# Kernel optimization log

Measured on AMD Instinct MI355X. Metric: run time of the kernel, lower is better.

Reference implementation:

```python
import jax, jax.numpy as jnp
import numpy as np

B, S, D, H = 2, 2048, 1024, 16
HD = D // H  # head_dim = 64


def setup_inputs() -> dict:
    key = jax.random.key(0)
    ks = jax.random.split(key, 5)
    scale = 1.0 / np.sqrt(D)
    return {
        "x": jax.random.normal(ks[0], (B, S, D), dtype=jnp.float32),
        "attention_mask": jnp.zeros((B, 1, 1, S), dtype=jnp.float32),
        "Wq": jax.random.normal(ks[1], (D, D), dtype=jnp.float32) * scale,
        "Wk": jax.random.normal(ks[2], (D, D), dtype=jnp.float32) * scale,
        "Wv": jax.random.normal(ks[3], (D, D), dtype=jnp.float32) * scale,
        "Wo": jax.random.normal(ks[4], (D, D), dtype=jnp.float32) * scale,
    }


def reference(x, attention_mask, Wq, Wk, Wv, Wo):
    # nn.Linear applies x @ W.T; weights here stored as [out, in]
    q = jnp.einsum("bsd,ed->bse", x, Wq).reshape(B, S, H, HD).transpose(0, 2, 1, 3)
    k = jnp.einsum("bsd,ed->bse", x, Wk).reshape(B, S, H, HD).transpose(0, 2, 1, 3)
    v = jnp.einsum("bsd,ed->bse", x, Wv).reshape(B, S, H, HD).transpose(0, 2, 1, 3)
    scores = jnp.einsum("bhqd,bhkd->bhqk", q, k) / jnp.sqrt(jnp.float32(HD))
    scores = scores + attention_mask  # additive mask, broadcasts [B,1,1,S]
    attn = jax.nn.softmax(scores, axis=-1)  # dropout p=0 (eval) -> identity
    ctx = jnp.einsum("bhqk,bhkd->bhqd", attn, v)
    ctx = ctx.transpose(0, 2, 1, 3).reshape(B, S, D)
    out = jnp.einsum("bsd,ed->bse", ctx, Wo)
    return out
```

## Files before the change

kernel.cpp:

```cpp
#include <hip/hip_runtime.h>
#include <hip/hip_bf16.h>
#include <cstdint>
#include <cstddef>


#define B_  2
#define S_  2048
#define D_  1024
#define H_  16
#define HD_ 64

typedef __bf16 bf16x8 __attribute__((ext_vector_type(8)));
typedef __bf16 bf16x4 __attribute__((ext_vector_type(4)));
typedef float  f32x4  __attribute__((ext_vector_type(4)));

__device__ __forceinline__ void async16(const __bf16* g, const __bf16* l) {
  __builtin_amdgcn_global_load_lds(
      (const __attribute__((address_space(1))) void*)(uintptr_t)g,
      (__attribute__((address_space(3))) void*)(uint32_t)(uintptr_t)l,
      16, 0, 0);
}

__global__ __launch_bounds__(256) void cvt_all(const float* __restrict__ x,
    const float* __restrict__ wq, const float* __restrict__ wk,
    const float* __restrict__ wv, const float* __restrict__ wo,
    __bf16* __restrict__ xb, __bf16* __restrict__ wqb, __bf16* __restrict__ wkb,
    __bf16* __restrict__ wvb, __bf16* __restrict__ wob) {
  const int sel = blockIdx.y;
  const float* src; __bf16* dst; int n;
  if      (sel == 0) { src = x;  dst = xb;  n = B_ * S_ * D_; }
  else if (sel == 1) { src = wq; dst = wqb; n = D_ * D_; }
  else if (sel == 2) { src = wk; dst = wkb; n = D_ * D_; }
  else if (sel == 3) { src = wv; dst = wvb; n = D_ * D_; }
  else               { src = wo; dst = wob; n = D_ * D_; }
  for (int i = blockIdx.x * 256 + threadIdx.x; i * 4 < n; i += gridDim.x * 256) {
    const float4 v = *(const float4*)(src + (size_t)i * 4);
    bf16x4 o;
    o[0] = (__bf16)v.x; o[1] = (__bf16)v.y; o[2] = (__bf16)v.z; o[3] = (__bf16)v.w;
    *(bf16x4*)(dst + (size_t)i * 4) = o;
  }
}

template <typename TC>
__device__ __forceinline__ void gemm97_body(const __bf16* __restrict__ A,
                                            const __bf16* __restrict__ Bm,
                                            TC* __restrict__ C,
                                            const int m0, const int n0,
                                            const int N, const int K) {
  __shared__ __align__(16) __bf16 As[128 * 64];
  __shared__ __align__(16) __bf16 Bs[128 * 64];
  const int tid  = threadIdx.x, lane = tid & 63, wave = tid >> 6;
  const int l15  = lane & 15,   quad = lane >> 4;
  const int wr   = wave >> 1,   wc   = wave & 1;
  const int ebase = wave * 2048 + lane * 8;

  f32x4 acc[4][4] = {};
  for (int k0 = 0; k0 < K; k0 += 64) {
#pragma unroll
    for (int i = 0; i < 4; ++i) {
      const int e = ebase + i * 512;
      const int row = e >> 6, col = e & 63;
      async16(A  + (size_t)(m0 + row) * K + k0 + col, As + (wave * 4 + i) * 512);
      async16(Bm + (size_t)(n0 + row) * K + k0 + col, Bs + (wave * 4 + i) * 512);
    }
    __syncthreads();
#pragma unroll
    for (int kk = 0; kk < 2; ++kk) {
      bf16x8 af[4], bfv[4];
#pragma unroll
      for (int rt = 0; rt < 4; ++rt)
        af[rt] = *(const bf16x8*)(As + (wr * 64 + rt * 16 + l15) * 64 + kk * 32 + quad * 8);
#pragma unroll
      for (int ct = 0; ct < 4; ++ct)
        bfv[ct] = *(const bf16x8*)(Bs + (wc * 64 + ct * 16 + l15) * 64 + kk * 32 + quad * 8);
#pragma unroll
      for (int rt = 0; rt < 4; ++rt)
#pragma unroll
        for (int ct = 0; ct < 4; ++ct)
          acc[rt][ct] = __builtin_amdgcn_mfma_f32_16x16x32_bf16(af[rt], bfv[ct], acc[rt][ct], 0, 0, 0);
    }
    __syncthreads();
  }
#pragma unroll
  for (int rt = 0; rt < 4; ++rt)
#pragma unroll
    for (int ct = 0; ct < 4; ++ct)
#pragma unroll
      for (int r = 0; r < 4; ++r) {
        const int row = m0 + wr * 64 + rt * 16 + quad * 4 + r;
        const int col = n0 + wc * 64 + ct * 16 + l15;
        C[(size_t)row * N + col] = (TC)acc[rt][ct][r];
      }
}

__global__ __launch_bounds__(256) void qkv_gemm(const __bf16* __restrict__ xb,
                                                const __bf16* __restrict__ wq,
                                                const __bf16* __restrict__ wk,
                                                const __bf16* __restrict__ wv,
                                                __bf16* __restrict__ qkv) {
  const int sel = blockIdx.x >> 3;
  const __bf16* Bm = (sel == 0) ? wq : (sel == 1) ? wk : wv;
  __bf16* C = qkv + (size_t)sel * ((size_t)B_ * S_ * D_);
  gemm97_body<__bf16>(xb, Bm, C, blockIdx.y * 128, (blockIdx.x & 7) * 128, D_, D_);
}

__global__ __launch_bounds__(256) void o_gemm(const __bf16* __restrict__ cb,
                                              const __bf16* __restrict__ wo,
                                              float* __restrict__ out) {
  gemm97_body<float>(cb, wo, out, blockIdx.y * 128, blockIdx.x * 128, D_, D_);
}

__global__ __launch_bounds__(256) void vtrans(const __bf16* __restrict__ vb,
                                              __bf16* __restrict__ vt) {
  __shared__ __bf16 tbuf[64][72];
  const int tid = threadIdx.x;
  const int s0 = blockIdx.x * 64, bh = blockIdx.y;
  const int b = bh >> 4, h = bh & 15;
  const __bf16* src = vb + ((size_t)b * S_ + s0) * D_ + h * HD_;
#pragma unroll
  for (int i = 0; i < 2; ++i) {
    const int r = i * 32 + (tid >> 3), c8 = (tid & 7) * 8;
    *(bf16x8*)(&tbuf[r][c8]) = *(const bf16x8*)(src + (size_t)r * D_ + c8);
  }
  __syncthreads();
  __bf16* dst = vt + (size_t)bh * HD_ * S_ + s0;
#pragma unroll
  for (int i = 0; i < 2; ++i) {
    const int hd = i * 32 + (tid >> 3), sc = (tid & 7) * 8;
    bf16x8 v;
#pragma unroll
    for (int j = 0; j < 8; ++j) v[j] = tbuf[sc + j][hd];
    *(bf16x8*)(dst + (size_t)hd * S_ + sc) = v;
  }
}

__global__ __launch_bounds__(256) void attn2(const __bf16* __restrict__ Q,
                                             const __bf16* __restrict__ K,
                                             const __bf16* __restrict__ Vt,
                                             const float* __restrict__ mask,
                                             __bf16* __restrict__ O) {
  constexpr int LKT = 72, LVT = 136, LPS = 136;
  __shared__ __align__(16) __bf16 kt[128 * LKT];
  __shared__ __align__(16) __bf16 vt[64 * LVT];
  __shared__ __align__(16) __bf16 ps[128 * LPS];
  __shared__ __align__(16) float  msk[128];

  const int tid  = threadIdx.x, lane = tid & 63, wave = tid >> 6;
  const int l15  = lane & 15,   quad = lane >> 4;
  const int b = blockIdx.z, h = blockIdx.y, q0 = blockIdx.x * 128;
  const size_t base   = (size_t)b * S_ * D_ + h * HD_;
  const size_t vtbase = (size_t)(b * H_ + h) * HD_ * S_;
  const int qw = q0 + wave * 32;

  bf16x8 qf[2][2];
#pragma unroll
  for (int t = 0; t < 2; ++t)
#pragma unroll
    for (int kb = 0; kb < 2; ++kb)
      qf[t][kb] = *(const bf16x8*)(Q + base + (size_t)(qw + t * 16 + l15) * D_ + kb * 32 + quad * 8);

  float m_run[2] = {-1e30f, -1e30f}, l_run[2] = {0.f, 0.f};
  f32x4 oacc[2][4] = {};

  for (int t0 = 0; t0 < S_; t0 += 128) {
    __syncthreads();
#pragma unroll
    for (int i = 0; i < 4; ++i) {
      const int idx = i * 256 + tid;
      { const int row = idx >> 3, c8 = (idx & 7) * 8;
        *(bf16x8*)(kt + row * LKT + c8) =
            *(const bf16x8*)(K + base + (size_t)(t0 + row) * D_ + c8); }
      { const int row = idx >> 4, c8 = (idx & 15) * 8;
        *(bf16x8*)(vt + row * LVT + c8) =
            *(const bf16x8*)(Vt + vtbase + (size_t)row * S_ + t0 + c8); }
    }
    if (tid < 128) msk[tid] = mask[(size_t)b * S_ + t0 + tid];
    __syncthreads();

    f32x4 sacc[8][2] = {};
#pragma unroll
    for (int kti = 0; kti < 8; ++kti) {
      const __bf16* kr = kt + (kti * 16 + l15) * LKT + quad * 8;
      const bf16x8 a0 = *(const bf16x8*)(kr);
      const bf16x8 a1 = *(const bf16x8*)(kr + 32);
#pragma unroll
      for (int t = 0; t < 2; ++t) {
        sacc[kti][t] = __builtin_amdgcn_mfma_f32_16x16x32_bf16(a0, qf[t][0], sacc[kti][t], 0, 0, 0);
        sacc[kti][t] = __builtin_amdgcn_mfma_f32_16x16x32_bf16(a1, qf[t][1], sacc[kti][t], 0, 0, 0);
      }
    }
#pragma unroll
    for (int kti = 0; kti < 8; ++kti) {
      const f32x4 mv = *(const f32x4*)(msk + kti * 16 + quad * 4);
#pragma unroll
      for (int t = 0; t < 2; ++t)
#pragma unroll
        for (int r = 0; r < 4; ++r)
          sacc[kti][t][r] = sacc[kti][t][r] * 0.125f + mv[r];
    }
    float mnew[2], alpha[2], tsum[2];
#pragma unroll
    for (int t = 0; t < 2; ++t) {
      float tm = -1e30f;
#pragma unroll
      for (int kti = 0; kti < 8; ++kti)
#pragma unroll
        for (int r = 0; r < 4; ++r) tm = fmaxf(tm, sacc[kti][t][r]);
      tm = fmaxf(tm, __shfl_xor(tm, 16));
      tm = fmaxf(tm, __shfl_xor(tm, 32));
      mnew[t]  = fmaxf(m_run[t], tm);
      alpha[t] = __expf(m_run[t] - mnew[t]);
      m_run[t] = mnew[t];
      tsum[t]  = 0.f;
    }
#pragma unroll
    for (int t = 0; t < 2; ++t) {
      __bf16* pr = ps + (size_t)(wave * 32 + t * 16 + l15) * LPS + quad * 4;
#pragma unroll
      for (int kti = 0; kti < 8; ++kti) {
        bf16x4 pv;
#pragma unroll
        for (int r = 0; r < 4; ++r) {
          const float p = __expf(sacc[kti][t][r] - mnew[t]);
          tsum[t] += p;
          pv[r] = (__bf16)p;
        }
        *(bf16x4*)(pr + kti * 16) = pv;
      }
    }
#pragma unroll
    for (int t = 0; t < 2; ++t) {
      float ts = tsum[t];
      ts += __shfl_xor(ts, 16);
      ts += __shfl_xor(ts, 32);
      l_run[t] = l_run[t] * alpha[t] + ts;
#pragma unroll
      for (int r = 0; r < 4; ++r) {
        const float aR = __shfl(alpha[t], quad * 4 + r);
#pragma unroll
        for (int nt = 0; nt < 4; ++nt) oacc[t][nt][r] *= aR;
      }
    }
#pragma unroll
    for (int kb = 0; kb < 4; ++kb) {
      bf16x8 pa[2];
#pragma unroll
      for (int t = 0; t < 2; ++t)
        pa[t] = *(const bf16x8*)(ps + (size_t)(wave * 32 + t * 16 + l15) * LPS + kb * 32 + quad * 8);
#pragma unroll
      for (int nt = 0; nt < 4; ++nt) {
        const bf16x8 vf = *(const bf16x8*)(vt + (nt * 16 + l15) * LVT + kb * 32 + quad * 8);
#pragma unroll
        for (int t = 0; t < 2; ++t)
          oacc[t][nt] = __builtin_amdgcn_mfma_f32_16x16x32_bf16(pa[t], vf, oacc[t][nt], 0, 0, 0);
      }
    }
  }
#pragma unroll
  for (int t = 0; t < 2; ++t)
#pragma unroll
    for (int r = 0; r < 4; ++r) {
      const float lR  = __shfl(l_run[t], quad * 4 + r);
      const float inv = 1.0f / lR;
      const int row = qw + t * 16 + quad * 4 + r;
#pragma unroll
      for (int nt = 0; nt < 4; ++nt)
        O[base + (size_t)row * D_ + nt * 16 + l15] = (__bf16)(oacc[t][nt][r] * inv);
    }
}

extern "C" void kernel_launch(void* const* d_in, const int* in_sizes, int n_in,
                              void* d_out, int out_size, void* d_ws, size_t ws_size,
                              hipStream_t stream) {
  const float* x    = (const float*)d_in[0];
  const float* mask = (const float*)d_in[1];
  const float* Wq   = (const float*)d_in[2];
  const float* Wk   = (const float*)d_in[3];
  const float* Wv   = (const float*)d_in[4];
  const float* Wo   = (const float*)d_in[5];

  char* ws = (char*)d_ws;
  const size_t MB = 1ull << 20;
  const size_t NT = (size_t)B_ * S_ * D_;
  __bf16* xb  = (__bf16*)(ws);
  __bf16* wqb = (__bf16*)(ws + 8 * MB);
  __bf16* wkb = (__bf16*)(ws + 10 * MB);
  __bf16* wvb = (__bf16*)(ws + 12 * MB);
  __bf16* wob = (__bf16*)(ws + 14 * MB);
  __bf16* qkv = (__bf16*)(ws + 16 * MB);
  __bf16* qb  = qkv;
  __bf16* kb  = qkv + NT;
  __bf16* vb  = qkv + 2 * NT;
  __bf16* vtb = xb;
  __bf16* cb  = vb;

  cvt_all<<<dim3(1024, 5), 256, 0, stream>>>(x, Wq, Wk, Wv, Wo, xb, wqb, wkb, wvb, wob);
  qkv_gemm<<<dim3(24, 32), 256, 0, stream>>>(xb, wqb, wkb, wvb, qkv);
  vtrans<<<dim3(32, 32), 256, 0, stream>>>(vb, vtb);
  attn2<<<dim3(S_ / 128, H_, B_), 256, 0, stream>>>(qb, kb, vtb, mask, cb);
  o_gemm<<<dim3(8, 32), 256, 0, stream>>>(cb, wob, (float*)d_out);
}
```

Measured before the change: 232.7 us.

## Load K/V/mask fragments directly from global in attention, use exp2 softmax

The attention kernel stops staging K, V^T and mask tiles in shared memory and has each wave load its MFMA operands straight from global memory, relying on L1/L2 caching across the four waves that share a block. Only the P tile stays in LDS, which cuts LDS use and may raise occupancy, and the cooperative copy with its barrier goes away. Softmax exponentials now use exp2 with a pre-multiplied log2(e) inside an fma. In exchange, each wave reissues global loads for the same K/V data, adding memory latency and traffic unless the cache absorbs it.

```diff
diff --git a/kernel.cpp b/kernel.cpp
--- a/kernel.cpp
+++ b/kernel.cpp
@@ -134,23 +134,22 @@
   }
 }
 
-__global__ __launch_bounds__(256) void attn2(const __bf16* __restrict__ Q,
+__global__ __launch_bounds__(256) void attn4(const __bf16* __restrict__ Q,
                                              const __bf16* __restrict__ K,
                                              const __bf16* __restrict__ Vt,
                                              const float* __restrict__ mask,
                                              __bf16* __restrict__ O) {
-  constexpr int LKT = 72, LVT = 136, LPS = 136;
-  __shared__ __align__(16) __bf16 kt[128 * LKT];
-  __shared__ __align__(16) __bf16 vt[64 * LVT];
+  constexpr int LPS = 136;
   __shared__ __align__(16) __bf16 ps[128 * LPS];
-  __shared__ __align__(16) float  msk[128];
 
   const int tid  = threadIdx.x, lane = tid & 63, wave = tid >> 6;
   const int l15  = lane & 15,   quad = lane >> 4;
   const int b = blockIdx.z, h = blockIdx.y, q0 = blockIdx.x * 128;
   const size_t base   = (size_t)b * S_ * D_ + h * HD_;
   const size_t vtbase = (size_t)(b * H_ + h) * HD_ * S_;
+  const float* mrow   = mask + (size_t)b * S_;
   const int qw = q0 + wave * 32;
+  const float L2E = 1.442695041f;
 
   bf16x8 qf[2][2];
 #pragma unroll
@@ -164,25 +163,12 @@
 
   for (int t0 = 0; t0 < S_; t0 += 128) {
     __syncthreads();
-#pragma unroll
-    for (int i = 0; i < 4; ++i) {
-      const int idx = i * 256 + tid;
-      { const int row = idx >> 3, c8 = (idx & 7) * 8;
-        *(bf16x8*)(kt + row * LKT + c8) =
-            *(const bf16x8*)(K + base + (size_t)(t0 + row) * D_ + c8); }
-      { const int row = idx >> 4, c8 = (idx & 15) * 8;
-        *(bf16x8*)(vt + row * LVT + c8) =
-            *(const bf16x8*)(Vt + vtbase + (size_t)row * S_ + t0 + c8); }
-    }
-    if (tid < 128) msk[tid] = mask[(size_t)b * S_ + t0 + tid];
-    __syncthreads();
-
     f32x4 sacc[8][2] = {};
 #pragma unroll
     for (int kti = 0; kti < 8; ++kti) {
-      const __bf16* kr = kt + (kti * 16 + l15) * LKT + quad * 8;
-      const bf16x8 a0 = *(const bf16x8*)(kr);
-      const bf16x8 a1 = *(const bf16x8*)(kr + 32);
+      const __bf16* kp = K + base + (size_t)(t0 + kti * 16 + l15) * D_ + quad * 8;
+      const bf16x8 a0 = *(const bf16x8*)(kp);
+      const bf16x8 a1 = *(const bf16x8*)(kp + 32);
 #pragma unroll
       for (int t = 0; t < 2; ++t) {
         sacc[kti][t] = __builtin_amdgcn_mfma_f32_16x16x32_bf16(a0, qf[t][0], sacc[kti][t], 0, 0, 0);
@@ -191,14 +177,14 @@
     }
 #pragma unroll
     for (int kti = 0; kti < 8; ++kti) {
-      const f32x4 mv = *(const f32x4*)(msk + kti * 16 + quad * 4);
+      const f32x4 mv = *(const f32x4*)(mrow + t0 + kti * 16 + quad * 4);
 #pragma unroll
       for (int t = 0; t < 2; ++t)
 #pragma unroll
         for (int r = 0; r < 4; ++r)
-          sacc[kti][t][r] = sacc[kti][t][r] * 0.125f + mv[r];
-    }
-    float mnew[2], alpha[2], tsum[2];
+          sacc[kti][t][r] = fmaf(sacc[kti][t][r], 0.125f, mv[r]);
+    }
+    float mnew[2], alpha[2], tsum[2], ml2[2];
 #pragma unroll
     for (int t = 0; t < 2; ++t) {
       float tm = -1e30f;
@@ -209,8 +195,9 @@
       tm = fmaxf(tm, __shfl_xor(tm, 16));
       tm = fmaxf(tm, __shfl_xor(tm, 32));
       mnew[t]  = fmaxf(m_run[t], tm);
-      alpha[t] = __expf(m_run[t] - mnew[t]);
+      alpha[t] = __builtin_amdgcn_exp2f((m_run[t] - mnew[t]) * L2E);
       m_run[t] = mnew[t];
+      ml2[t]   = mnew[t] * L2E;
       tsum[t]  = 0.f;
     }
 #pragma unroll
@@ -221,7 +208,7 @@
         bf16x4 pv;
 #pragma unroll
         for (int r = 0; r < 4; ++r) {
-          const float p = __expf(sacc[kti][t][r] - mnew[t]);
+          const float p = __builtin_amdgcn_exp2f(fmaf(sacc[kti][t][r], L2E, -ml2[t]));
           tsum[t] += p;
           pv[r] = (__bf16)p;
         }
@@ -241,6 +228,7 @@
         for (int nt = 0; nt < 4; ++nt) oacc[t][nt][r] *= aR;
       }
     }
+    __syncthreads();
 #pragma unroll
     for (int kb = 0; kb < 4; ++kb) {
       bf16x8 pa[2];
@@ -249,7 +237,7 @@
         pa[t] = *(const bf16x8*)(ps + (size_t)(wave * 32 + t * 16 + l15) * LPS + kb * 32 + quad * 8);
 #pragma unroll
       for (int nt = 0; nt < 4; ++nt) {
-        const bf16x8 vf = *(const bf16x8*)(vt + (nt * 16 + l15) * LVT + kb * 32 + quad * 8);
+        const bf16x8 vf = *(const bf16x8*)(Vt + vtbase + (size_t)(nt * 16 + l15) * S_ + t0 + kb * 32 + quad * 8);
 #pragma unroll
         for (int t = 0; t < 2; ++t)
           oacc[t][nt] = __builtin_amdgcn_mfma_f32_16x16x32_bf16(pa[t], vf, oacc[t][nt], 0, 0, 0);
@@ -297,6 +285,6 @@
   cvt_all<<<dim3(1024, 5), 256, 0, stream>>>(x, Wq, Wk, Wv, Wo, xb, wqb, wkb, wvb, wob);
   qkv_gemm<<<dim3(24, 32), 256, 0, stream>>>(xb, wqb, wkb, wvb, qkv);
   vtrans<<<dim3(32, 32), 256, 0, stream>>>(vb, vtb);
-  attn2<<<dim3(S_ / 128, H_, B_), 256, 0, stream>>>(qb, kb, vtb, mask, cb);
+  attn4<<<dim3(S_ / 128, H_, B_), 256, 0, stream>>>(qb, kb, vtb, mask, cb);
   o_gemm<<<dim3(8, 32), 256, 0, stream>>>(cb, wob, (float*)d_out);
 }
```

Result: slower. 320.2 us (+37.6%).
